# Performance work log

Hardware: AMD Instinct MI355X
Metric: run time of the kernel (lower is better)

Reference implementation:

```python
import jax, jax.numpy as jnp
import numpy as np

N = 40000      # nodes
E = 640000     # edges (avg degree 16)
F = 128        # in_feats
OUT = 128      # out_feats


def setup_inputs() -> dict:
    key = jax.random.key(0)
    ks = jax.random.split(key, 8)
    feat = jax.random.normal(ks[0], (N, F), dtype=jnp.float32)
    src = jax.random.randint(ks[1], (E,), 0, N, dtype=jnp.int32)
    dst = jnp.sort(jax.random.randint(ks[2], (E,), 0, N, dtype=jnp.int32))
    # AttentionAGG: fc1 (2F -> F), fc2 (F -> 1); fc_layer (2F -> OUT)
    s1 = 1.0 / np.sqrt(2 * F)
    s2 = 1.0 / np.sqrt(F)
    w1 = jax.random.normal(ks[3], (2 * F, F), dtype=jnp.float32) * s1
    b1 = jnp.zeros((F,), dtype=jnp.float32)
    w2 = jax.random.normal(ks[4], (F, 1), dtype=jnp.float32) * s2
    b2 = jnp.zeros((1,), dtype=jnp.float32)
    wf = jax.random.normal(ks[5], (2 * F, OUT), dtype=jnp.float32) * s1
    bf = jnp.zeros((OUT,), dtype=jnp.float32)
    return {"feat": feat, "src": src, "dst": dst,
            "w1": w1, "b1": b1, "w2": w2, "b2": b2, "wf": wf, "bf": bf}


def reference(feat, src, dst, w1, b1, w2, b2, wf, bf):
    f = feat.shape[1]
    n = feat.shape[0]
    # fc1(concat(h_dst, m_src)) == h_dst @ w1[:F] + h_src @ w1[F:]  (edge_weight is None)
    proj_dst = feat @ w1[:f]          # [N, F]
    proj_src = feat @ w1[f:]          # [N, F]
    pre = jnp.tanh(proj_dst[dst] + proj_src[src] + b1)   # [E, F]
    scores = (pre @ w2)[:, 0] + b2[0]                    # [E]
    # softmax over the ragged incoming-edge set of each dst node
    smax = jax.ops.segment_max(scores, dst, num_segments=n, indices_are_sorted=True)
    ex = jnp.exp(scores - jax.lax.stop_gradient(smax)[dst])
    den = jax.ops.segment_sum(ex, dst, num_segments=n, indices_are_sorted=True)
    att = ex / den[dst]                                  # [E]
    # weighted segment-sum of messages (m_e = feat[src]); zero-degree nodes get 0
    neigh = jax.ops.segment_sum(att[:, None] * feat[src], dst,
                                num_segments=n, indices_are_sorted=True)  # [N, F]
    # fc_layer(concat(h_self, neigh))
    rst = feat @ wf[:f] + neigh @ wf[f:] + bf            # [N, OUT]
    return rst
```

## Files before the change

### kernel.cpp

```cpp
#include <hip/hip_runtime.h>
#include <math.h>

#define F 128
#define OUT 128

typedef unsigned short ushort_t;
typedef __attribute__((ext_vector_type(8))) short bfrag;
typedef __attribute__((ext_vector_type(4))) float ffrag;

__device__ __forceinline__ float bf_lo(unsigned int u) {
    return __uint_as_float(u << 16);
}
__device__ __forceinline__ float bf_hi(unsigned int u) {
    return __uint_as_float(u & 0xffff0000u);
}
__device__ __forceinline__ ushort_t f2bf(float f) {
    unsigned int x = __float_as_uint(f);
    unsigned int r = x + 0x7fffu + ((x >> 16) & 1u);
    return (ushort_t)(r >> 16);
}
__device__ __forceinline__ unsigned pk2(float lo, float hi) {
    return (unsigned)f2bf(lo) | ((unsigned)f2bf(hi) << 16);
}

__global__ __launch_bounds__(256) void prep_kernel(
    const float* __restrict__ feat, const float* __restrict__ w1,
    const float* __restrict__ wf, const int* __restrict__ dst,
    ushort_t* __restrict__ abig, ushort_t* __restrict__ srcpack,
    ushort_t* __restrict__ btp, ushort_t* __restrict__ btf,
    int* __restrict__ row_ptr, int n, int e, int nb0, int nb1, int nb2)
{
    const int b = blockIdx.x, t = threadIdx.x;
    if (b < nb0) {
        int i = b * 256 + t;
        if (i >= n * 16) return;
        int row = i >> 4, c = (i & 15) * 8;
        float4 a = *(const float4*)(feat + (size_t)row * F + c);
        float4 bb = *(const float4*)(feat + (size_t)row * F + c + 4);
        unsigned p0 = pk2(a.x, a.y), p1 = pk2(a.z, a.w);
        unsigned p2 = pk2(bb.x, bb.y), p3 = pk2(bb.z, bb.w);
        *(uint4*)(abig + (size_t)row * 256 + c) = make_uint4(p0, p1, p2, p3);
        *(uint2*)(srcpack + (size_t)row * 256 + c * 2 + 4) = make_uint2(p0, p1);
        *(uint2*)(srcpack + (size_t)row * 256 + c * 2 + 12) = make_uint2(p2, p3);
    } else if (b < nb0 + nb1) {
        int idx = (b - nb0) * 256 + t;
        int j = idx >> 7, k = idx & 127;
        float v = (j < F) ? w1[(size_t)k * F + j]
                          : w1[(size_t)(F + k) * F + (j - F)];
        btp[idx] = f2bf(v);
    } else if (b < nb0 + nb1 + nb2) {
        int idx = (b - nb0 - nb1) * 256 + t;
        int j = idx >> 8, k = idx & 255;
        btf[idx] = f2bf(wf[(size_t)k * F + j]);
    } else {
        int i = (b - nb0 - nb1 - nb2) * 256 + t;
        if (i >= e) return;
        int d = dst[i];
        int prev = (i == 0) ? -1 : dst[i - 1];
        for (int v = prev + 1; v <= d; ++v) row_ptr[v] = i;
        if (i == e - 1) {
            for (int v = d + 1; v <= n; ++v) row_ptr[v] = e;
        }
    }
}

#define PST 136
__global__ __launch_bounds__(256) void proj_gemm_kernel(
    const ushort_t* __restrict__ abig, const ushort_t* __restrict__ btp,
    const float* __restrict__ b1, ushort_t* __restrict__ e_dst,
    ushort_t* __restrict__ srcpack, int n)
{
    __shared__ ushort_t As[64 * PST];
    __shared__ ushort_t Ep[4][16 * 80];
    const int t = threadIdx.x;
    const int wv = t >> 6, lane = t & 63;
    const int lm = lane & 15, quad = lane >> 4;
    const int row0 = blockIdx.x * 64, col0 = wv * 64;

#pragma unroll
    for (int k = 0; k < 4; ++k) {
        int l = k * 256 + t;
        int r = l >> 4, ch = l & 15;
        uint4 d = make_uint4(0, 0, 0, 0);
        if (row0 + r < n) d = *(const uint4*)(abig + (size_t)(row0 + r) * 256 + ch * 8);
        *(uint4*)(As + r * PST + ch * 8) = d;
    }
    __syncthreads();

    bfrag bfr[4][4];
#pragma unroll
    for (int ks = 0; ks < 4; ++ks)
#pragma unroll
        for (int ni = 0; ni < 4; ++ni)
            bfr[ks][ni] = *(const bfrag*)(btp + (size_t)(col0 + ni * 16 + lm) * 128
                                          + ks * 32 + quad * 8);

    ffrag acc[4][4];
#pragma unroll
    for (int mi = 0; mi < 4; ++mi)
#pragma unroll
        for (int ni = 0; ni < 4; ++ni) acc[mi][ni] = (ffrag){0.f, 0.f, 0.f, 0.f};

#pragma unroll
    for (int ks = 0; ks < 4; ++ks)
#pragma unroll
        for (int mi = 0; mi < 4; ++mi) {
            bfrag af = *(const bfrag*)(As + (mi * 16 + lm) * PST + ks * 32 + quad * 8);
#pragma unroll
            for (int ni = 0; ni < 4; ++ni)
                acc[mi][ni] = __builtin_amdgcn_mfma_f32_16x16x32_bf16(
                    af, bfr[ks][ni], acc[mi][ni], 0, 0, 0);
        }

    float bias[4];
#pragma unroll
    for (int ni = 0; ni < 4; ++ni)
        bias[ni] = (col0 < F) ? b1[col0 + ni * 16 + lm] : 0.f;

#pragma unroll
    for (int mi = 0; mi < 4; ++mi) {
#pragma unroll
        for (int ni = 0; ni < 4; ++ni)
#pragma unroll
            for (int r = 0; r < 4; ++r)
                Ep[wv][(quad * 4 + r) * 80 + ni * 16 + lm] =
                    f2bf(__expf(2.f * (acc[mi][ni][r] + bias[ni])));
#pragma unroll
        for (int ps = 0; ps < 2; ++ps) {
            int rl = ps * 8 + (lane >> 3), co = (lane & 7) * 8;
            uint4 vv = *(const uint4*)(&Ep[wv][rl * 80 + co]);
            int grow = row0 + mi * 16 + rl;
            if (grow < n) {
                if (col0 < F) {
                    *(uint4*)(e_dst + (size_t)grow * F + col0 + co) = vv;
                } else {
                    int f0 = col0 - F + co;
                    *(uint2*)(srcpack + (size_t)grow * 256 + f0 * 2) =
                        make_uint2(vv.x, vv.y);
                    *(uint2*)(srcpack + (size_t)grow * 256 + f0 * 2 + 8) =
                        make_uint2(vv.z, vv.w);
                }
            }
        }
    }
}

__global__ __launch_bounds__(256) void fused_kernel(
    const ushort_t* __restrict__ e_dst, const ushort_t* __restrict__ srcpack,
    const int* __restrict__ src, const int* __restrict__ row_ptr,
    const float* __restrict__ w2, ushort_t* __restrict__ abig, int n)
{
    const int v = (int)((blockIdx.x * 256u + threadIdx.x) >> 5);
    const int fl = threadIdx.x & 31;
    const int sbase = threadIdx.x & 32;

    const float4 wv4 = ((const float4*)w2)[fl];
    const float w0 = wv4.x, w1_ = wv4.y, w2_ = wv4.z, w3_ = wv4.w;
    float sw = w0 + w1_ + w2_ + w3_;
    float aw = fabsf(w0) + fabsf(w1_) + fabsf(w2_) + fabsf(w3_);
#pragma unroll
    for (int off = 16; off; off >>= 1) {
        sw += __shfl_xor(sw, off, 64);
        aw += __shfl_xor(aw, off, 64);
    }
    const float K = sw - aw;

    if (v >= n) return;
    const int begin = row_ptr[v], end = row_ptr[v + 1];

    const uint2 ud = *(const uint2*)(e_dst + (size_t)v * F + fl * 4);
    const float ea0 = bf_lo(ud.x), ea1 = bf_hi(ud.x);
    const float ea2 = bf_lo(ud.y), ea3 = bf_hi(ud.y);

    float s = 0.f, a0 = 0.f, a1 = 0.f, a2 = 0.f, a3 = 0.f;

    for (int cb = begin; cb < end; cb += 32) {
        const int clen = min(32, end - cb);
        const int sv = (fl < clen) ? src[cb + fl] : 0;
        int jj = 0;
        for (; jj + 4 <= clen; jj += 4) {
            uint4 u[4];
#pragma unroll
            for (int q = 0; q < 4; ++q) {
                const int sq = __shfl(sv, sbase + jj + q, 64);
                u[q] = ((const uint4*)(srcpack + (size_t)sq * 256))[fl];
            }
            float p[4];
#pragma unroll
            for (int q = 0; q < 4; ++q) {
                float r;
                r = __builtin_amdgcn_rcpf(fmaf(ea0, bf_lo(u[q].x), 1.f)); p[q] = w0 * r;
                r = __builtin_amdgcn_rcpf(fmaf(ea1, bf_hi(u[q].x), 1.f)); p[q] = fmaf(w1_, r, p[q]);
                r = __builtin_amdgcn_rcpf(fmaf(ea2, bf_lo(u[q].y), 1.f)); p[q] = fmaf(w2_, r, p[q]);
                r = __builtin_amdgcn_rcpf(fmaf(ea3, bf_hi(u[q].y), 1.f)); p[q] = fmaf(w3_, r, p[q]);
            }
#pragma unroll
            for (int off = 16; off; off >>= 1) {
#pragma unroll
                for (int q = 0; q < 4; ++q) p[q] += __shfl_xor(p[q], off, 64);
            }
            float g[4];
#pragma unroll
            for (int q = 0; q < 4; ++q) g[q] = __expf(fmaf(-2.f, p[q], K));
            s += (g[0] + g[1]) + (g[2] + g[3]);
#pragma unroll
            for (int q = 0; q < 4; ++q) {
                a0 = fmaf(g[q], bf_lo(u[q].z), a0);
                a1 = fmaf(g[q], bf_hi(u[q].z), a1);
                a2 = fmaf(g[q], bf_lo(u[q].w), a2);
                a3 = fmaf(g[q], bf_hi(u[q].w), a3);
            }
        }
        for (; jj < clen; ++jj) {
            const int s0 = __shfl(sv, sbase + jj, 64);
            const uint4 u0 = ((const uint4*)(srcpack + (size_t)s0 * 256))[fl];
            float r, p0;
            r = __builtin_amdgcn_rcpf(fmaf(ea0, bf_lo(u0.x), 1.f)); p0 = w0 * r;
            r = __builtin_amdgcn_rcpf(fmaf(ea1, bf_hi(u0.x), 1.f)); p0 = fmaf(w1_, r, p0);
            r = __builtin_amdgcn_rcpf(fmaf(ea2, bf_lo(u0.y), 1.f)); p0 = fmaf(w2_, r, p0);
            r = __builtin_amdgcn_rcpf(fmaf(ea3, bf_hi(u0.y), 1.f)); p0 = fmaf(w3_, r, p0);
#pragma unroll
            for (int off = 16; off; off >>= 1) p0 += __shfl_xor(p0, off, 64);
            const float g0 = __expf(fmaf(-2.f, p0, K));
            s += g0;
            a0 = fmaf(g0, bf_lo(u0.z), a0);
            a1 = fmaf(g0, bf_hi(u0.z), a1);
            a2 = fmaf(g0, bf_lo(u0.w), a2);
            a3 = fmaf(g0, bf_hi(u0.w), a3);
        }
    }

    const float inv = (end > begin) ? 1.f / s : 0.f;
    ushort4 o = make_ushort4(f2bf(a0 * inv), f2bf(a1 * inv),
                             f2bf(a2 * inv), f2bf(a3 * inv));
    *(ushort4*)(abig + (size_t)v * 256 + 128 + fl * 4) = o;
}

#define OST 280
__global__ __launch_bounds__(256) void out_gemm_kernel(
    const ushort_t* __restrict__ abig, const ushort_t* __restrict__ btf,
    const float* __restrict__ bfv, float* __restrict__ out, int n)
{
    __shared__ ushort_t As[64 * OST];
    const int t = threadIdx.x;
    const int wv = t >> 6, lane = t & 63;
    const int lm = lane & 15, quad = lane >> 4;
    const int row0 = blockIdx.x * 64, col0 = wv * 32;

#pragma unroll
    for (int k = 0; k < 8; ++k) {
        int l = k * 256 + t;
        int r = l >> 5, ch = l & 31;
        uint4 d = make_uint4(0, 0, 0, 0);
        if (row0 + r < n) d = *(const uint4*)(abig + (size_t)(row0 + r) * 256 + ch * 8);
        *(uint4*)(As + r * OST + ch * 8) = d;
    }
    __syncthreads();

    bfrag bfr[8][2];
#pragma unroll
    for (int ks = 0; ks < 8; ++ks)
#pragma unroll
        for (int ni = 0; ni < 2; ++ni)
            bfr[ks][ni] = *(const bfrag*)(btf + (size_t)(col0 + ni * 16 + lm) * 256
                                          + ks * 32 + quad * 8);

    ffrag acc[4][2];
#pragma unroll
    for (int mi = 0; mi < 4; ++mi)
#pragma unroll
        for (int ni = 0; ni < 2; ++ni) acc[mi][ni] = (ffrag){0.f, 0.f, 0.f, 0.f};

#pragma unroll
    for (int ks = 0; ks < 8; ++ks)
#pragma unroll
        for (int mi = 0; mi < 4; ++mi) {
            bfrag af = *(const bfrag*)(As + (mi * 16 + lm) * OST + ks * 32 + quad * 8);
#pragma unroll
            for (int ni = 0; ni < 2; ++ni)
                acc[mi][ni] = __builtin_amdgcn_mfma_f32_16x16x32_bf16(
                    af, bfr[ks][ni], acc[mi][ni], 0, 0, 0);
        }

#pragma unroll
    for (int ni = 0; ni < 2; ++ni) {
        const int j = col0 + ni * 16 + lm;
        const float bb = bfv[j];
#pragma unroll
        for (int mi = 0; mi < 4; ++mi)
#pragma unroll
            for (int r = 0; r < 4; ++r) {
                int grow = row0 + mi * 16 + quad * 4 + r;
                if (grow < n) out[(size_t)grow * OUT + j] = acc[mi][ni][r] + bb;
            }
    }
}

extern "C" void kernel_launch(void* const* d_in, const int* in_sizes, int n_in,
                              void* d_out, int out_size, void* d_ws, size_t ws_size,
                              hipStream_t stream)
{
    const float* feat = (const float*)d_in[0];
    const int*   src  = (const int*)d_in[1];
    const int*   dst  = (const int*)d_in[2];
    const float* w1   = (const float*)d_in[3];
    const float* b1   = (const float*)d_in[4];
    const float* w2   = (const float*)d_in[5];
    const float* b2   = (const float*)d_in[6];  (void)b2;
    const float* wf   = (const float*)d_in[7];
    const float* bfv  = (const float*)d_in[8];
    float* out = (float*)d_out;

    const int n = in_sizes[0] / F;
    const int e = in_sizes[1];

    ushort_t* abig    = (ushort_t*)d_ws;
    ushort_t* e_dst   = abig + (size_t)n * 256;
    ushort_t* srcpack = e_dst + (size_t)n * 128;
    ushort_t* btp     = srcpack + (size_t)n * 256;
    ushort_t* btf     = btp + 32768;
    int* row_ptr      = (int*)(btf + 32768);

    const int nb0 = (n * 16 + 255) / 256;
    const int nb1 = 128, nb2 = 128;
    const int nb3 = (e + 255) / 256;

    prep_kernel<<<nb0 + nb1 + nb2 + nb3, 256, 0, stream>>>(
        feat, w1, wf, dst, abig, srcpack, btp, btf, row_ptr, n, e, nb0, nb1, nb2);
    proj_gemm_kernel<<<(n + 63) / 64, 256, 0, stream>>>(
        abig, btp, b1, e_dst, srcpack, n);
    fused_kernel<<<(n + 7) / 8, 256, 0, stream>>>(
        e_dst, srcpack, src, row_ptr, w2, abig, n);
    out_gemm_kernel<<<(n + 63) / 64, 256, 0, stream>>>(abig, btf, bfv, out, n);
}
```

Before: 170.1 us.

## Shrink GEMM row tiles to 16 and move srcpack feature interleave into proj GEMM

Both GEMM kernels now process 16 rows per block instead of 64, which quadruples the block count for better occupancy and latency hiding but reloads the B weight fragments four times as often. The barrier is moved after the weight fragment loads so those global loads overlap the shared-memory fill. The prep kernel no longer writes the bf16 feature half of srcpack; the proj GEMM writes whole 16-byte interleaved srcpack chunks from its staged A tile, replacing scattered 8-byte stores. The out GEMM's shared-memory row stride is also reduced.

New measurement: 180.9 us. 6.4% more time.

```diff
diff --git a/kernel.cpp b/kernel.cpp
--- a/kernel.cpp
+++ b/kernel.cpp
@@ -26,9 +26,9 @@
 __global__ __launch_bounds__(256) void prep_kernel(
     const float* __restrict__ feat, const float* __restrict__ w1,
     const float* __restrict__ wf, const int* __restrict__ dst,
-    ushort_t* __restrict__ abig, ushort_t* __restrict__ srcpack,
-    ushort_t* __restrict__ btp, ushort_t* __restrict__ btf,
-    int* __restrict__ row_ptr, int n, int e, int nb0, int nb1, int nb2)
+    ushort_t* __restrict__ abig, ushort_t* __restrict__ btp,
+    ushort_t* __restrict__ btf, int* __restrict__ row_ptr,
+    int n, int e, int nb0, int nb1, int nb2)
 {
     const int b = blockIdx.x, t = threadIdx.x;
     if (b < nb0) {
@@ -37,11 +37,8 @@
         int row = i >> 4, c = (i & 15) * 8;
         float4 a = *(const float4*)(feat + (size_t)row * F + c);
         float4 bb = *(const float4*)(feat + (size_t)row * F + c + 4);
-        unsigned p0 = pk2(a.x, a.y), p1 = pk2(a.z, a.w);
-        unsigned p2 = pk2(bb.x, bb.y), p3 = pk2(bb.z, bb.w);
-        *(uint4*)(abig + (size_t)row * 256 + c) = make_uint4(p0, p1, p2, p3);
-        *(uint2*)(srcpack + (size_t)row * 256 + c * 2 + 4) = make_uint2(p0, p1);
-        *(uint2*)(srcpack + (size_t)row * 256 + c * 2 + 12) = make_uint2(p2, p3);
+        *(uint4*)(abig + (size_t)row * 256 + c) =
+            make_uint4(pk2(a.x, a.y), pk2(a.z, a.w), pk2(bb.x, bb.y), pk2(bb.z, bb.w));
     } else if (b < nb0 + nb1) {
         int idx = (b - nb0) * 256 + t;
         int j = idx >> 7, k = idx & 127;
@@ -70,22 +67,19 @@
     const float* __restrict__ b1, ushort_t* __restrict__ e_dst,
     ushort_t* __restrict__ srcpack, int n)
 {
-    __shared__ ushort_t As[64 * PST];
+    __shared__ ushort_t As[16 * PST];
     __shared__ ushort_t Ep[4][16 * 80];
     const int t = threadIdx.x;
     const int wv = t >> 6, lane = t & 63;
     const int lm = lane & 15, quad = lane >> 4;
-    const int row0 = blockIdx.x * 64, col0 = wv * 64;
-
-#pragma unroll
-    for (int k = 0; k < 4; ++k) {
-        int l = k * 256 + t;
-        int r = l >> 4, ch = l & 15;
+    const int row0 = blockIdx.x * 16, col0 = wv * 64;
+
+    {
+        int r = t >> 4, ch = t & 15;
         uint4 d = make_uint4(0, 0, 0, 0);
         if (row0 + r < n) d = *(const uint4*)(abig + (size_t)(row0 + r) * 256 + ch * 8);
         *(uint4*)(As + r * PST + ch * 8) = d;
     }
-    __syncthreads();
 
     bfrag bfr[4][4];
 #pragma unroll
@@ -94,23 +88,20 @@
         for (int ni = 0; ni < 4; ++ni)
             bfr[ks][ni] = *(const bfrag*)(btp + (size_t)(col0 + ni * 16 + lm) * 128
                                           + ks * 32 + quad * 8);
-
-    ffrag acc[4][4];
-#pragma unroll
-    for (int mi = 0; mi < 4; ++mi)
-#pragma unroll
-        for (int ni = 0; ni < 4; ++ni) acc[mi][ni] = (ffrag){0.f, 0.f, 0.f, 0.f};
-
-#pragma unroll
-    for (int ks = 0; ks < 4; ++ks)
-#pragma unroll
-        for (int mi = 0; mi < 4; ++mi) {
-            bfrag af = *(const bfrag*)(As + (mi * 16 + lm) * PST + ks * 32 + quad * 8);
-#pragma unroll
-            for (int ni = 0; ni < 4; ++ni)
-                acc[mi][ni] = __builtin_amdgcn_mfma_f32_16x16x32_bf16(
-                    af, bfr[ks][ni], acc[mi][ni], 0, 0, 0);
-        }
+    __syncthreads();
+
+    ffrag acc[4];
+#pragma unroll
+    for (int ni = 0; ni < 4; ++ni) acc[ni] = (ffrag){0.f, 0.f, 0.f, 0.f};
+
+#pragma unroll
+    for (int ks = 0; ks < 4; ++ks) {
+        bfrag af = *(const bfrag*)(As + lm * PST + ks * 32 + quad * 8);
+#pragma unroll
+        for (int ni = 0; ni < 4; ++ni)
+            acc[ni] = __builtin_amdgcn_mfma_f32_16x16x32_bf16(
+                af, bfr[ks][ni], acc[ni], 0, 0, 0);
+    }
 
     float bias[4];
 #pragma unroll
@@ -118,29 +109,34 @@
         bias[ni] = (col0 < F) ? b1[col0 + ni * 16 + lm] : 0.f;
 
 #pragma unroll
-    for (int mi = 0; mi < 4; ++mi) {
-#pragma unroll
-        for (int ni = 0; ni < 4; ++ni)
-#pragma unroll
-            for (int r = 0; r < 4; ++r)
-                Ep[wv][(quad * 4 + r) * 80 + ni * 16 + lm] =
-                    f2bf(__expf(2.f * (acc[mi][ni][r] + bias[ni])));
+    for (int ni = 0; ni < 4; ++ni)
+#pragma unroll
+        for (int r = 0; r < 4; ++r)
+            Ep[wv][(quad * 4 + r) * 80 + ni * 16 + lm] =
+                f2bf(__expf(2.f * (acc[ni][r] + bias[ni])));
+
+    if (col0 < F) {
 #pragma unroll
         for (int ps = 0; ps < 2; ++ps) {
             int rl = ps * 8 + (lane >> 3), co = (lane & 7) * 8;
             uint4 vv = *(const uint4*)(&Ep[wv][rl * 80 + co]);
-            int grow = row0 + mi * 16 + rl;
-            if (grow < n) {
-                if (col0 < F) {
-                    *(uint4*)(e_dst + (size_t)grow * F + col0 + co) = vv;
-                } else {
-                    int f0 = col0 - F + co;
-                    *(uint2*)(srcpack + (size_t)grow * 256 + f0 * 2) =
-                        make_uint2(vv.x, vv.y);
-                    *(uint2*)(srcpack + (size_t)grow * 256 + f0 * 2 + 8) =
-                        make_uint2(vv.z, vv.w);
-                }
-            }
+            int grow = row0 + rl;
+            if (grow < n)
+                *(uint4*)(e_dst + (size_t)grow * F + col0 + co) = vv;
+        }
+    } else {
+        const int cbase = (col0 - F) >> 2;
+#pragma unroll
+        for (int ps = 0; ps < 4; ++ps) {
+            int rl = ps * 4 + (lane >> 4);
+            int c  = lane & 15;
+            int cg = cbase + c;
+            uint2 es = *(const uint2*)(&Ep[wv][rl * 80 + c * 4]);
+            uint2 ft = *(const uint2*)(As + rl * PST + cg * 4);
+            int grow = row0 + rl;
+            if (grow < n)
+                *(uint4*)(srcpack + (size_t)grow * 256 + cg * 8) =
+                    make_uint4(es.x, es.y, ft.x, ft.y);
         }
     }
 }
@@ -236,26 +232,25 @@
     *(ushort4*)(abig + (size_t)v * 256 + 128 + fl * 4) = o;
 }
 
-#define OST 280
+#define OST 264
 __global__ __launch_bounds__(256) void out_gemm_kernel(
     const ushort_t* __restrict__ abig, const ushort_t* __restrict__ btf,
     const float* __restrict__ bfv, float* __restrict__ out, int n)
 {
-    __shared__ ushort_t As[64 * OST];
+    __shared__ ushort_t As[16 * OST];
     const int t = threadIdx.x;
     const int wv = t >> 6, lane = t & 63;
     const int lm = lane & 15, quad = lane >> 4;
-    const int row0 = blockIdx.x * 64, col0 = wv * 32;
-
-#pragma unroll
-    for (int k = 0; k < 8; ++k) {
+    const int row0 = blockIdx.x * 16, col0 = wv * 32;
+
+#pragma unroll
+    for (int k = 0; k < 2; ++k) {
         int l = k * 256 + t;
         int r = l >> 5, ch = l & 31;
         uint4 d = make_uint4(0, 0, 0, 0);
         if (row0 + r < n) d = *(const uint4*)(abig + (size_t)(row0 + r) * 256 + ch * 8);
         *(uint4*)(As + r * OST + ch * 8) = d;
     }
-    __syncthreads();
 
     bfrag bfr[8][2];
 #pragma unroll
@@ -264,35 +259,30 @@
         for (int ni = 0; ni < 2; ++ni)
             bfr[ks][ni] = *(const bfrag*)(btf + (size_t)(col0 + ni * 16 + lm) * 256
                                           + ks * 32 + quad * 8);
-
-    ffrag acc[4][2];
-#pragma unroll
-    for (int mi = 0; mi < 4; ++mi)
-#pragma unroll
-        for (int ni = 0; ni < 2; ++ni) acc[mi][ni] = (ffrag){0.f, 0.f, 0.f, 0.f};
-
-#pragma unroll
-    for (int ks = 0; ks < 8; ++ks)
-#pragma unroll
-        for (int mi = 0; mi < 4; ++mi) {
-            bfrag af = *(const bfrag*)(As + (mi * 16 + lm) * OST + ks * 32 + quad * 8);
-#pragma unroll
-            for (int ni = 0; ni < 2; ++ni)
-                acc[mi][ni] = __builtin_amdgcn_mfma_f32_16x16x32_bf16(
-                    af, bfr[ks][ni], acc[mi][ni], 0, 0, 0);
-        }
+    __syncthreads();
+
+    ffrag acc[2];
+#pragma unroll
+    for (int ni = 0; ni < 2; ++ni) acc[ni] = (ffrag){0.f, 0.f, 0.f, 0.f};
+
+#pragma unroll
+    for (int ks = 0; ks < 8; ++ks) {
+        bfrag af = *(const bfrag*)(As + lm * OST + ks * 32 + quad * 8);
+#pragma unroll
+        for (int ni = 0; ni < 2; ++ni)
+            acc[ni] = __builtin_amdgcn_mfma_f32_16x16x32_bf16(
+                af, bfr[ks][ni], acc[ni], 0, 0, 0);
+    }
 
 #pragma unroll
     for (int ni = 0; ni < 2; ++ni) {
         const int j = col0 + ni * 16 + lm;
         const float bb = bfv[j];
 #pragma unroll
-        for (int mi = 0; mi < 4; ++mi)
-#pragma unroll
-            for (int r = 0; r < 4; ++r) {
-                int grow = row0 + mi * 16 + quad * 4 + r;
-                if (grow < n) out[(size_t)grow * OUT + j] = acc[mi][ni][r] + bb;
-            }
+        for (int r = 0; r < 4; ++r) {
+            int grow = row0 + quad * 4 + r;
+            if (grow < n) out[(size_t)grow * OUT + j] = acc[ni][r] + bb;
+        }
     }
 }
 
@@ -326,10 +316,10 @@
     const int nb3 = (e + 255) / 256;
 
     prep_kernel<<<nb0 + nb1 + nb2 + nb3, 256, 0, stream>>>(
-        feat, w1, wf, dst, abig, srcpack, btp, btf, row_ptr, n, e, nb0, nb1, nb2);
-    proj_gemm_kernel<<<(n + 63) / 64, 256, 0, stream>>>(
+        feat, w1, wf, dst, abig, btp, btf, row_ptr, n, e, nb0, nb1, nb2);
+    proj_gemm_kernel<<<(n + 15) / 16, 256, 0, stream>>>(
         abig, btp, b1, e_dst, srcpack, n);
     fused_kernel<<<(n + 7) / 8, 256, 0, stream>>>(
         e_dst, srcpack, src, row_ptr, w2, abig, n);
-    out_gemm_kernel<<<(n + 63) / 64, 256, 0, stream>>>(abig, btf, bfv, out, n);
-}
+    out_gemm_kernel<<<(n + 15) / 16, 256, 0, stream>>>(abig, btf, bfv, out, n);
+}
```

## Fuse all four stages into one persistent cooperative kernel with grid syncs

Applied to the files above, without the earlier changes.

Replaces the four separate launches (prep, projection GEMM, edge attention aggregation, output GEMM) with a single cooperative persistent kernel that uses grid.sync between stages. This removes launch gaps and inter-kernel drain. It also moves packing of source features into srcpack from prep into the projection GEMM epilogue, so they are written together with the projected values. The risks are smaller 16-row GEMM tiles that reload B fragments from global memory per tile, a grid capped at 1024 blocks with occupancy limits, and grid-sync overhead. If the cooperative launch fails, the old multi-kernel path runs instead.

Result: slower. 387.4 us (+127.7%).

```diff
diff --git a/kernel.cpp b/kernel.cpp
--- a/kernel.cpp
+++ b/kernel.cpp
@@ -1,8 +1,14 @@
 #include <hip/hip_runtime.h>
+#include <hip/hip_cooperative_groups.h>
 #include <math.h>
+
+namespace cg = cooperative_groups;
 
 #define F 128
 #define OUT 128
+#define PST 136
+#define GOST 264
+#define FOST 280
 
 typedef unsigned short ushort_t;
 typedef __attribute__((ext_vector_type(8))) short bfrag;
@@ -23,12 +29,245 @@
     return (unsigned)f2bf(lo) | ((unsigned)f2bf(hi) << 16);
 }
 
+__global__ __launch_bounds__(256, 4) void giga_kernel(
+    const float* __restrict__ feat, const float* __restrict__ w1,
+    const float* __restrict__ b1, const float* __restrict__ w2,
+    const float* __restrict__ wf, const float* __restrict__ bfv,
+    const int* __restrict__ src, const int* __restrict__ dst,
+    float* __restrict__ out,
+    ushort_t* __restrict__ abig, ushort_t* __restrict__ e_dst,
+    ushort_t* __restrict__ srcpack, ushort_t* __restrict__ btp,
+    ushort_t* __restrict__ btf, int* __restrict__ row_ptr,
+    int n, int e)
+{
+    cg::grid_group grid = cg::this_grid();
+    const int nb = gridDim.x;
+    const int b = blockIdx.x, t = threadIdx.x;
+    const int wv = t >> 6, lane = t & 63;
+    const int lm = lane & 15, quad = lane >> 4;
+
+    __shared__ __align__(16) unsigned char smem[16384];
+    ushort_t* As = (ushort_t*)smem;
+    ushort_t* Ep = (ushort_t*)(smem + 4352);
+
+    for (int i = b * 256 + t; i < n * 16; i += nb * 256) {
+        int row = i >> 4, c = (i & 15) * 8;
+        float4 a = *(const float4*)(feat + (size_t)row * F + c);
+        float4 bb = *(const float4*)(feat + (size_t)row * F + c + 4);
+        *(uint4*)(abig + (size_t)row * 256 + c) =
+            make_uint4(pk2(a.x, a.y), pk2(a.z, a.w), pk2(bb.x, bb.y), pk2(bb.z, bb.w));
+    }
+    for (int idx = b * 256 + t; idx < 32768; idx += nb * 256) {
+        int j = idx >> 7, k = idx & 127;
+        float v = (j < F) ? w1[(size_t)k * F + j]
+                          : w1[(size_t)(F + k) * F + (j - F)];
+        btp[idx] = f2bf(v);
+    }
+    for (int idx = b * 256 + t; idx < 32768; idx += nb * 256) {
+        int j = idx >> 8, k = idx & 255;
+        btf[idx] = f2bf(wf[(size_t)k * F + j]);
+    }
+    for (int i = b * 256 + t; i < e; i += nb * 256) {
+        int d = dst[i];
+        int prev = (i == 0) ? -1 : dst[i - 1];
+        for (int v = prev + 1; v <= d; ++v) row_ptr[v] = i;
+        if (i == e - 1) {
+            for (int v = d + 1; v <= n; ++v) row_ptr[v] = e;
+        }
+    }
+    grid.sync();
+
+    const int ntile = (n + 15) / 16;
+    const int col0 = wv * 64;
+    for (int tile = b; tile < ntile; tile += nb) {
+        const int row0 = tile * 16;
+        {
+            int r = t >> 4, ch = t & 15;
+            uint4 d = *(const uint4*)(abig + (size_t)(row0 + r) * 256 + ch * 8);
+            *(uint4*)(As + r * PST + ch * 8) = d;
+        }
+        __syncthreads();
+
+        ffrag acc[4];
+#pragma unroll
+        for (int ni = 0; ni < 4; ++ni) acc[ni] = (ffrag){0.f, 0.f, 0.f, 0.f};
+#pragma unroll
+        for (int ks = 0; ks < 4; ++ks) {
+            bfrag af = *(const bfrag*)(As + lm * PST + ks * 32 + quad * 8);
+#pragma unroll
+            for (int ni = 0; ni < 4; ++ni) {
+                bfrag bv = *(const bfrag*)(btp + (size_t)(col0 + ni * 16 + lm) * 128
+                                           + ks * 32 + quad * 8);
+                acc[ni] = __builtin_amdgcn_mfma_f32_16x16x32_bf16(af, bv, acc[ni], 0, 0, 0);
+            }
+        }
+
+#pragma unroll
+        for (int ni = 0; ni < 4; ++ni) {
+            const float bias = (col0 < F) ? b1[col0 + ni * 16 + lm] : 0.f;
+#pragma unroll
+            for (int r = 0; r < 4; ++r)
+                Ep[wv * 1280 + (quad * 4 + r) * 80 + ni * 16 + lm] =
+                    f2bf(__expf(2.f * (acc[ni][r] + bias)));
+        }
+
+        if (col0 < F) {
+#pragma unroll
+            for (int ps = 0; ps < 2; ++ps) {
+                int rl = ps * 8 + (lane >> 3), co = (lane & 7) * 8;
+                uint4 vv = *(const uint4*)(&Ep[wv * 1280 + rl * 80 + co]);
+                *(uint4*)(e_dst + (size_t)(row0 + rl) * F + col0 + co) = vv;
+            }
+        } else {
+            const int cbase = (col0 - F) >> 2;
+#pragma unroll
+            for (int ps = 0; ps < 4; ++ps) {
+                int rl = ps * 4 + (lane >> 4);
+                int c  = lane & 15;
+                int cg2 = cbase + c;
+                uint2 es = *(const uint2*)(&Ep[wv * 1280 + rl * 80 + c * 4]);
+                uint2 ft = *(const uint2*)(As + rl * PST + cg2 * 4);
+                *(uint4*)(srcpack + (size_t)(row0 + rl) * 256 + cg2 * 8) =
+                    make_uint4(es.x, es.y, ft.x, ft.y);
+            }
+        }
+        __syncthreads();
+    }
+    grid.sync();
+
+    {
+        const int fl = t & 31;
+        const int sbase = t & 32;
+        const float4 wv4 = ((const float4*)w2)[fl];
+        const float w0 = wv4.x, w1_ = wv4.y, w2_ = wv4.z, w3_ = wv4.w;
+        float sw = w0 + w1_ + w2_ + w3_;
+        float aw = fabsf(w0) + fabsf(w1_) + fabsf(w2_) + fabsf(w3_);
+#pragma unroll
+        for (int off = 16; off; off >>= 1) {
+            sw += __shfl_xor(sw, off, 64);
+            aw += __shfl_xor(aw, off, 64);
+        }
+        const float K = sw - aw;
+
+        const int ngrp = (n + 7) / 8;
+        for (int g = b; g < ngrp; g += nb) {
+            const int v = g * 8 + (t >> 5);
+            const int begin = row_ptr[v], end = row_ptr[v + 1];
+
+            const uint2 ud = *(const uint2*)(e_dst + (size_t)v * F + fl * 4);
+            const float ea0 = bf_lo(ud.x), ea1 = bf_hi(ud.x);
+            const float ea2 = bf_lo(ud.y), ea3 = bf_hi(ud.y);
+
+            float s = 0.f, a0 = 0.f, a1 = 0.f, a2 = 0.f, a3 = 0.f;
+
+            for (int cb = begin; cb < end; cb += 32) {
+                const int clen = min(32, end - cb);
+                const int sv = (fl < clen) ? src[cb + fl] : 0;
+                int jj = 0;
+                for (; jj + 4 <= clen; jj += 4) {
+                    uint4 u[4];
+#pragma unroll
+                    for (int q = 0; q < 4; ++q) {
+                        const int sq = __shfl(sv, sbase + jj + q, 64);
+                        u[q] = ((const uint4*)(srcpack + (size_t)sq * 256))[fl];
+                    }
+                    float p[4];
+#pragma unroll
+                    for (int q = 0; q < 4; ++q) {
+                        float r;
+                        r = __builtin_amdgcn_rcpf(fmaf(ea0, bf_lo(u[q].x), 1.f)); p[q] = w0 * r;
+                        r = __builtin_amdgcn_rcpf(fmaf(ea1, bf_hi(u[q].x), 1.f)); p[q] = fmaf(w1_, r, p[q]);
+                        r = __builtin_amdgcn_rcpf(fmaf(ea2, bf_lo(u[q].y), 1.f)); p[q] = fmaf(w2_, r, p[q]);
+                        r = __builtin_amdgcn_rcpf(fmaf(ea3, bf_hi(u[q].y), 1.f)); p[q] = fmaf(w3_, r, p[q]);
+                    }
+#pragma unroll
+                    for (int off = 16; off; off >>= 1) {
+#pragma unroll
+                        for (int q = 0; q < 4; ++q) p[q] += __shfl_xor(p[q], off, 64);
+                    }
+                    float gq[4];
+#pragma unroll
+                    for (int q = 0; q < 4; ++q) gq[q] = __expf(fmaf(-2.f, p[q], K));
+                    s += (gq[0] + gq[1]) + (gq[2] + gq[3]);
+#pragma unroll
+                    for (int q = 0; q < 4; ++q) {
+                        a0 = fmaf(gq[q], bf_lo(u[q].z), a0);
+                        a1 = fmaf(gq[q], bf_hi(u[q].z), a1);
+                        a2 = fmaf(gq[q], bf_lo(u[q].w), a2);
+                        a3 = fmaf(gq[q], bf_hi(u[q].w), a3);
+                    }
+                }
+                for (; jj < clen; ++jj) {
+                    const int s0 = __shfl(sv, sbase + jj, 64);
+                    const uint4 u0 = ((const uint4*)(srcpack + (size_t)s0 * 256))[fl];
+                    float r, p0;
+                    r = __builtin_amdgcn_rcpf(fmaf(ea0, bf_lo(u0.x), 1.f)); p0 = w0 * r;
+                    r = __builtin_amdgcn_rcpf(fmaf(ea1, bf_hi(u0.x), 1.f)); p0 = fmaf(w1_, r, p0);
+                    r = __builtin_amdgcn_rcpf(fmaf(ea2, bf_lo(u0.y), 1.f)); p0 = fmaf(w2_, r, p0);
+                    r = __builtin_amdgcn_rcpf(fmaf(ea3, bf_hi(u0.y), 1.f)); p0 = fmaf(w3_, r, p0);
+#pragma unroll
+                    for (int off = 16; off; off >>= 1) p0 += __shfl_xor(p0, off, 64);
+                    const float g0 = __expf(fmaf(-2.f, p0, K));
+                    s += g0;
+                    a0 = fmaf(g0, bf_lo(u0.z), a0);
+                    a1 = fmaf(g0, bf_hi(u0.z), a1);
+                    a2 = fmaf(g0, bf_lo(u0.w), a2);
+                    a3 = fmaf(g0, bf_hi(u0.w), a3);
+                }
+            }
+
+            const float inv = (end > begin) ? 1.f / s : 0.f;
+            *(ushort4*)(abig + (size_t)v * 256 + 128 + fl * 4) =
+                make_ushort4(f2bf(a0 * inv), f2bf(a1 * inv),
+                             f2bf(a2 * inv), f2bf(a3 * inv));
+        }
+    }
+    grid.sync();
+
+    const int col0g = wv * 32;
+    for (int tile = b; tile < ntile; tile += nb) {
+        const int row0 = tile * 16;
+#pragma unroll
+        for (int k = 0; k < 2; ++k) {
+            int l = k * 256 + t;
+            int r = l >> 5, ch = l & 31;
+            uint4 d = *(const uint4*)(abig + (size_t)(row0 + r) * 256 + ch * 8);
+            *(uint4*)(As + r * GOST + ch * 8) = d;
+        }
+        __syncthreads();
+
+        ffrag acc[2];
+#pragma unroll
+        for (int ni = 0; ni < 2; ++ni) acc[ni] = (ffrag){0.f, 0.f, 0.f, 0.f};
+#pragma unroll
+        for (int ks = 0; ks < 8; ++ks) {
+            bfrag af = *(const bfrag*)(As + lm * GOST + ks * 32 + quad * 8);
+#pragma unroll
+            for (int ni = 0; ni < 2; ++ni) {
+                bfrag bv = *(const bfrag*)(btf + (size_t)(col0g + ni * 16 + lm) * 256
+                                           + ks * 32 + quad * 8);
+                acc[ni] = __builtin_amdgcn_mfma_f32_16x16x32_bf16(af, bv, acc[ni], 0, 0, 0);
+            }
+        }
+
+#pragma unroll
+        for (int ni = 0; ni < 2; ++ni) {
+            const int j = col0g + ni * 16 + lm;
+            const float bb = bfv[j];
+#pragma unroll
+            for (int r = 0; r < 4; ++r)
+                out[(size_t)(row0 + quad * 4 + r) * OUT + j] = acc[ni][r] + bb;
+        }
+        __syncthreads();
+    }
+}
+
 __global__ __launch_bounds__(256) void prep_kernel(
     const float* __restrict__ feat, const float* __restrict__ w1,
     const float* __restrict__ wf, const int* __restrict__ dst,
-    ushort_t* __restrict__ abig, ushort_t* __restrict__ srcpack,
-    ushort_t* __restrict__ btp, ushort_t* __restrict__ btf,
-    int* __restrict__ row_ptr, int n, int e, int nb0, int nb1, int nb2)
+    ushort_t* __restrict__ abig, ushort_t* __restrict__ btp,
+    ushort_t* __restrict__ btf, int* __restrict__ row_ptr,
+    int n, int e, int nb0, int nb1, int nb2)
 {
     const int b = blockIdx.x, t = threadIdx.x;
     if (b < nb0) {
@@ -37,11 +276,8 @@
         int row = i >> 4, c = (i & 15) * 8;
         float4 a = *(const float4*)(feat + (size_t)row * F + c);
         float4 bb = *(const float4*)(feat + (size_t)row * F + c + 4);
-        unsigned p0 = pk2(a.x, a.y), p1 = pk2(a.z, a.w);
-        unsigned p2 = pk2(bb.x, bb.y), p3 = pk2(bb.z, bb.w);
-        *(uint4*)(abig + (size_t)row * 256 + c) = make_uint4(p0, p1, p2, p3);
-        *(uint2*)(srcpack + (size_t)row * 256 + c * 2 + 4) = make_uint2(p0, p1);
-        *(uint2*)(srcpack + (size_t)row * 256 + c * 2 + 12) = make_uint2(p2, p3);
+        *(uint4*)(abig + (size_t)row * 256 + c) =
+            make_uint4(pk2(a.x, a.y), pk2(a.z, a.w), pk2(bb.x, bb.y), pk2(bb.z, bb.w));
     } else if (b < nb0 + nb1) {
         int idx = (b - nb0) * 256 + t;
         int j = idx >> 7, k = idx & 127;
@@ -64,7 +300,6 @@
     }
 }
 
-#define PST 136
 __global__ __launch_bounds__(256) void proj_gemm_kernel(
     const ushort_t* __restrict__ abig, const ushort_t* __restrict__ btp,
     const float* __restrict__ b1, ushort_t* __restrict__ e_dst,
@@ -125,21 +360,29 @@
             for (int r = 0; r < 4; ++r)
                 Ep[wv][(quad * 4 + r) * 80 + ni * 16 + lm] =
                     f2bf(__expf(2.f * (acc[mi][ni][r] + bias[ni])));
-#pragma unroll
-        for (int ps = 0; ps < 2; ++ps) {
-            int rl = ps * 8 + (lane >> 3), co = (lane & 7) * 8;
-            uint4 vv = *(const uint4*)(&Ep[wv][rl * 80 + co]);
-            int grow = row0 + mi * 16 + rl;
-            if (grow < n) {
-                if (col0 < F) {
+
+        if (col0 < F) {
+#pragma unroll
+            for (int ps = 0; ps < 2; ++ps) {
+                int rl = ps * 8 + (lane >> 3), co = (lane & 7) * 8;
+                uint4 vv = *(const uint4*)(&Ep[wv][rl * 80 + co]);
+                int grow = row0 + mi * 16 + rl;
+                if (grow < n)
                     *(uint4*)(e_dst + (size_t)grow * F + col0 + co) = vv;
-                } else {
-                    int f0 = col0 - F + co;
-                    *(uint2*)(srcpack + (size_t)grow * 256 + f0 * 2) =
-                        make_uint2(vv.x, vv.y);
-                    *(uint2*)(srcpack + (size_t)grow * 256 + f0 * 2 + 8) =
-                        make_uint2(vv.z, vv.w);
-                }
+            }
+        } else {
+            const int cbase = (col0 - F) >> 2;
+#pragma unroll
+            for (int ps = 0; ps < 4; ++ps) {
+                int rl = ps * 4 + (lane >> 4);
+                int c  = lane & 15;
+                int cg2 = cbase + c;
+                uint2 es = *(const uint2*)(&Ep[wv][rl * 80 + c * 4]);
+                uint2 ft = *(const uint2*)(As + (mi * 16 + rl) * PST + cg2 * 4);
+                int grow = row0 + mi * 16 + rl;
+                if (grow < n)
+                    *(uint4*)(srcpack + (size_t)grow * 256 + cg2 * 8) =
+                        make_uint4(es.x, es.y, ft.x, ft.y);
             }
         }
     }
@@ -231,17 +474,15 @@
     }
 
     const float inv = (end > begin) ? 1.f / s : 0.f;
-    ushort4 o = make_ushort4(f2bf(a0 * inv), f2bf(a1 * inv),
-                             f2bf(a2 * inv), f2bf(a3 * inv));
-    *(ushort4*)(abig + (size_t)v * 256 + 128 + fl * 4) = o;
-}
-
-#define OST 280
+    *(ushort4*)(abig + (size_t)v * 256 + 128 + fl * 4) =
+        make_ushort4(f2bf(a0 * inv), f2bf(a1 * inv), f2bf(a2 * inv), f2bf(a3 * inv));
+}
+
 __global__ __launch_bounds__(256) void out_gemm_kernel(
     const ushort_t* __restrict__ abig, const ushort_t* __restrict__ btf,
     const float* __restrict__ bfv, float* __restrict__ out, int n)
 {
-    __shared__ ushort_t As[64 * OST];
+    __shared__ ushort_t As[64 * FOST];
     const int t = threadIdx.x;
     const int wv = t >> 6, lane = t & 63;
     const int lm = lane & 15, quad = lane >> 4;
@@ -253,7 +494,7 @@
         int r = l >> 5, ch = l & 31;
         uint4 d = make_uint4(0, 0, 0, 0);
         if (row0 + r < n) d = *(const uint4*)(abig + (size_t)(row0 + r) * 256 + ch * 8);
-        *(uint4*)(As + r * OST + ch * 8) = d;
+        *(uint4*)(As + r * FOST + ch * 8) = d;
     }
     __syncthreads();
 
@@ -275,7 +516,7 @@
     for (int ks = 0; ks < 8; ++ks)
 #pragma unroll
         for (int mi = 0; mi < 4; ++mi) {
-            bfrag af = *(const bfrag*)(As + (mi * 16 + lm) * OST + ks * 32 + quad * 8);
+            bfrag af = *(const bfrag*)(As + (mi * 16 + lm) * FOST + ks * 32 + quad * 8);
 #pragma unroll
             for (int ni = 0; ni < 2; ++ni)
                 acc[mi][ni] = __builtin_amdgcn_mfma_f32_16x16x32_bf16(
@@ -311,8 +552,8 @@
     const float* bfv  = (const float*)d_in[8];
     float* out = (float*)d_out;
 
-    const int n = in_sizes[0] / F;
-    const int e = in_sizes[1];
+    int n = in_sizes[0] / F;
+    int e = in_sizes[1];
 
     ushort_t* abig    = (ushort_t*)d_ws;
     ushort_t* e_dst   = abig + (size_t)n * 256;
@@ -321,12 +562,29 @@
     ushort_t* btf     = btp + 32768;
     int* row_ptr      = (int*)(btf + 32768);
 
+    hipError_t lerr = hipErrorUnknown;
+    int maxPerCU = 0;
+    hipError_t qerr = hipOccupancyMaxActiveBlocksPerMultiprocessor(
+        &maxPerCU, giga_kernel, 256, 0);
+    if (qerr == hipSuccess && maxPerCU > 0) {
+        int grid = maxPerCU * 256;
+        if (grid > 1024) grid = 1024;
+        void* args[] = {
+            (void*)&feat, (void*)&w1, (void*)&b1, (void*)&w2, (void*)&wf,
+            (void*)&bfv, (void*)&src, (void*)&dst, (void*)&out,
+            (void*)&abig, (void*)&e_dst, (void*)&srcpack, (void*)&btp,
+            (void*)&btf, (void*)&row_ptr, (void*)&n, (void*)&e
+        };
+        lerr = hipLaunchCooperativeKernel((void*)giga_kernel, dim3(grid),
+                                          dim3(256), args, 0, stream);
+    }
+    if (lerr == hipSuccess) return;
+
     const int nb0 = (n * 16 + 255) / 256;
     const int nb1 = 128, nb2 = 128;
     const int nb3 = (e + 255) / 256;
-
     prep_kernel<<<nb0 + nb1 + nb2 + nb3, 256, 0, stream>>>(
-        feat, w1, wf, dst, abig, srcpack, btp, btf, row_ptr, n, e, nb0, nb1, nb2);
+        feat, w1, wf, dst, abig, btp, btf, row_ptr, n, e, nb0, nb1, nb2);
     proj_gemm_kernel<<<(n + 63) / 64, 256, 0, stream>>>(
         abig, btp, b1, e_dst, srcpack, n);
     fused_kernel<<<(n + 7) / 8, 256, 0, stream>>>(
```
